# Performance work log

Measured on AMD Instinct MI355X. Metric: run time of the kernel, lower is better.

## Reference

```python
import jax, jax.numpy as jnp
import numpy as np
from jax import lax

IMAGE_SIZE = (224, 224)
NUM_NN = 3
SIGMA = 4


def _gaussian_kernel1d(sigma: float) -> jnp.ndarray:
    # anomalib/kornia: kernel_size = 2 * int(4.0 * sigma + 0.5) + 1
    ksize = 2 * int(4.0 * sigma + 0.5) + 1
    x = jnp.arange(ksize, dtype=jnp.float32) - ksize // 2
    g = jnp.exp(-(x * x) / (2.0 * sigma * sigma))
    return g / jnp.sum(g)


def _gaussian_blur(x: jnp.ndarray, sigma: float) -> jnp.ndarray:
    # x: [B, 1, H, W]; reflect 'same' padding + separable depthwise conv
    g = _gaussian_kernel1d(sigma)
    k = g.shape[0]
    pad = k // 2
    x = jnp.pad(x, ((0, 0), (0, 0), (pad, pad), (pad, pad)), mode='reflect')
    dn = ('NCHW', 'OIHW', 'NCHW')
    x = lax.conv_general_dilated(x, g.reshape(1, 1, k, 1), (1, 1), 'VALID', dimension_numbers=dn)
    x = lax.conv_general_dilated(x, g.reshape(1, 1, 1, k), (1, 1), 'VALID', dimension_numbers=dn)
    return x


def setup_inputs() -> dict:
    key = jax.random.key(0)
    distance = jax.random.uniform(key, (16, 3136, 4096), dtype=jnp.float32)
    return {"distance": distance, "scale_h": 56, "scale_w": 56}


def reference(distance, scale_h, scale_w):
    b = distance.shape[0]
    d = jnp.sqrt(distance)                                   # [B, HW, M]
    # topk smallest (ascending), like torch.topk(largest=False)
    vals = -lax.top_k(-d, NUM_NN)[0]                         # [B, HW, K]
    w = jax.nn.softmax(-vals, axis=-1)                       # softmin
    s = w[:, :, 0] * vals[:, :, 0]                           # [B, HW]
    score = s.reshape(b, 1, scale_h, scale_w)                # 'b (h w) c -> b c h w', c=1
    score = lax.stop_gradient(score)                         # .detach()
    amap = jnp.mean(score, axis=1, keepdims=True)            # [B, 1, h, w]
    amap = jax.image.resize(amap, (b, 1, IMAGE_SIZE[0], IMAGE_SIZE[1]), method='bilinear')
    return _gaussian_blur(amap, SIGMA)
```

## Files before the change

### kernel.cpp

```cpp
#include <hip/hip_runtime.h>

#define NB   16
#define HW   3136
#define MEL  4096
#define SH   56
#define SW   56
#define OH   224
#define OW   224
#define KRAD 16
#define NPIX (NB * OH * OW)

__device__ __forceinline__ void ins3(float v, float& m0, float& m1, float& m2) {
    float a = fminf(v, m0);
    float b = fmaxf(v, m0);
    m0 = a;
    float c = fminf(b, m1);
    float d = fmaxf(b, m1);
    m1 = c;
    m2 = fminf(d, m2);
}

__global__ __launch_bounds__(256) void topk_score_kernel(const float* __restrict__ dist,
                                                         float* __restrict__ score) {
    const int wid  = threadIdx.x >> 6;
    const int lane = threadIdx.x & 63;
    const long long row = (long long)blockIdx.x * 4 + wid;
    const float4* p = (const float4*)(dist + row * (long long)MEL);

    float a0 = 3.4e38f, a1 = 3.4e38f, a2 = 3.4e38f;
    float b0 = 3.4e38f, b1 = 3.4e38f, b2 = 3.4e38f;

    #pragma unroll 4
    for (int j = 0; j < 16; ++j) {
        float4 v = p[lane + 64 * j];
        ins3(v.x, a0, a1, a2);
        ins3(v.y, b0, b1, b2);
        ins3(v.z, a0, a1, a2);
        ins3(v.w, b0, b1, b2);
    }
    ins3(b0, a0, a1, a2);
    ins3(b1, a0, a1, a2);
    ins3(b2, a0, a1, a2);

    #pragma unroll
    for (int off = 32; off > 0; off >>= 1) {
        float s0 = __shfl_xor(a0, off);
        float s1 = __shfl_xor(a1, off);
        float s2 = __shfl_xor(a2, off);
        ins3(s0, a0, a1, a2);
        ins3(s1, a0, a1, a2);
        ins3(s2, a0, a1, a2);
    }

    if (lane == 0) {
        float v0 = sqrtf(a0), v1 = sqrtf(a1), v2 = sqrtf(a2);
        float e1 = expf(v0 - v1);
        float e2 = expf(v0 - v2);
        score[row] = v0 / (1.0f + e1 + e2);
    }
}

__global__ void init_gauss_kernel(float* __restrict__ g) {
    __shared__ float t[2 * KRAD + 1];
    int i = threadIdx.x;
    if (i < 2 * KRAD + 1) {
        float k = (float)(i - KRAD);
        t[i] = expf(-k * k * (1.0f / 32.0f));
    }
    __syncthreads();
    if (i == 0) {
        float s = 0.0f;
        for (int j = 0; j < 2 * KRAD + 1; ++j) s += t[j];
        for (int j = 0; j < 2 * KRAD + 1; ++j) g[j] = t[j] / s;
    }
}

__global__ __launch_bounds__(256) void upsample_kernel(const float* __restrict__ score,
                                                       float* __restrict__ out) {
    int idx = blockIdx.x * 256 + threadIdx.x;
    if (idx >= NPIX) return;
    int ox = idx % OW;
    int t  = idx / OW;
    int oy = t % OH;
    int b  = t / OH;

    float sx = (ox + 0.5f) * 0.25f - 0.5f;
    float sy = (oy + 0.5f) * 0.25f - 0.5f;
    sx = fmaxf(sx, 0.0f);
    sy = fmaxf(sy, 0.0f);
    int x0 = (int)sx;
    int y0 = (int)sy;
    float fx = sx - (float)x0;
    float fy = sy - (float)y0;
    int x1 = min(x0 + 1, SW - 1);
    int y1 = min(y0 + 1, SH - 1);

    const float* s = score + b * (SH * SW);
    float v00 = s[y0 * SW + x0];
    float v01 = s[y0 * SW + x1];
    float v10 = s[y1 * SW + x0];
    float v11 = s[y1 * SW + x1];
    float r0 = v00 + (v01 - v00) * fx;
    float r1 = v10 + (v11 - v10) * fx;
    out[idx] = r0 + (r1 - r0) * fy;
}

__global__ __launch_bounds__(256) void blur_v_kernel(const float* __restrict__ in,
                                                     const float* __restrict__ g,
                                                     float* __restrict__ out) {
    int idx = blockIdx.x * 256 + threadIdx.x;
    if (idx >= NPIX) return;
    int x = idx % OW;
    int t = idx / OW;
    int y = t % OH;
    const float* img = in + (long long)(t - y) * OW;

    float acc = 0.0f;
    #pragma unroll
    for (int k = -KRAD; k <= KRAD; ++k) {
        int yy = y + k;
        yy = (yy < 0) ? -yy : yy;
        yy = (yy > OH - 1) ? (2 * (OH - 1) - yy) : yy;
        acc += g[k + KRAD] * img[yy * OW + x];
    }
    out[idx] = acc;
}

__global__ __launch_bounds__(256) void blur_h_kernel(const float* __restrict__ in,
                                                     const float* __restrict__ g,
                                                     float* __restrict__ out) {
    int idx = blockIdx.x * 256 + threadIdx.x;
    if (idx >= NPIX) return;
    int x = idx % OW;
    const float* rowp = in + (idx - x);

    float acc = 0.0f;
    #pragma unroll
    for (int k = -KRAD; k <= KRAD; ++k) {
        int xx = x + k;
        xx = (xx < 0) ? -xx : xx;
        xx = (xx > OW - 1) ? (2 * (OW - 1) - xx) : xx;
        acc += g[k + KRAD] * rowp[xx];
    }
    out[idx] = acc;
}

extern "C" void kernel_launch(void* const* d_in, const int* in_sizes, int n_in,
                              void* d_out, int out_size, void* d_ws, size_t ws_size,
                              hipStream_t stream) {
    const float* dist = (const float*)d_in[0];
    float* out = (float*)d_out;

    char* ws = (char*)d_ws;
    float* score = (float*)ws;
    float* gauss = (float*)(ws + 50176 * 4);
    float* tmp   = (float*)(ws + 262144);

    init_gauss_kernel<<<1, 64, 0, stream>>>(gauss);
    topk_score_kernel<<<(NB * HW) / 4, 256, 0, stream>>>(dist, score);
    upsample_kernel<<<NPIX / 256, 256, 0, stream>>>(score, out);
    blur_v_kernel<<<NPIX / 256, 256, 0, stream>>>(out, gauss, tmp);
    blur_h_kernel<<<NPIX / 256, 256, 0, stream>>>(tmp, gauss, out);
}
```

Before: 171.8 us.

## Fuse upsample and separable blur into one kernel, batch nontemporal loads in top-k

The gaussian init, bilinear upsample, vertical blur and horizontal blur are merged into a single post kernel with one block per output row. Each block recomputes the upsampled values it needs straight from the small score map and keeps the row in shared memory for the horizontal pass. This removes three launches and the full-resolution intermediate buffers. The top-k kernel now issues all sixteen vector loads up front as nontemporal loads, which adds memory-level parallelism at the cost of more registers.

```diff
diff --git a/kernel.cpp b/kernel.cpp
--- a/kernel.cpp
+++ b/kernel.cpp
@@ -9,6 +9,8 @@
 #define OW   224
 #define KRAD 16
 #define NPIX (NB * OH * OW)
+
+typedef float vf4 __attribute__((ext_vector_type(4)));
 
 __device__ __forceinline__ void ins3(float v, float& m0, float& m1, float& m2) {
     float a = fminf(v, m0);
@@ -25,18 +27,22 @@
     const int wid  = threadIdx.x >> 6;
     const int lane = threadIdx.x & 63;
     const long long row = (long long)blockIdx.x * 4 + wid;
-    const float4* p = (const float4*)(dist + row * (long long)MEL);
+    const vf4* p = (const vf4*)(dist + row * (long long)MEL);
+
+    vf4 v[16];
+    #pragma unroll
+    for (int j = 0; j < 16; ++j)
+        v[j] = __builtin_nontemporal_load(p + lane + 64 * j);
 
     float a0 = 3.4e38f, a1 = 3.4e38f, a2 = 3.4e38f;
     float b0 = 3.4e38f, b1 = 3.4e38f, b2 = 3.4e38f;
 
-    #pragma unroll 4
+    #pragma unroll
     for (int j = 0; j < 16; ++j) {
-        float4 v = p[lane + 64 * j];
-        ins3(v.x, a0, a1, a2);
-        ins3(v.y, b0, b1, b2);
-        ins3(v.z, a0, a1, a2);
-        ins3(v.w, b0, b1, b2);
+        ins3(v[j][0], a0, a1, a2);
+        ins3(v[j][1], b0, b1, b2);
+        ins3(v[j][2], a0, a1, a2);
+        ins3(v[j][3], b0, b1, b2);
     }
     ins3(b0, a0, a1, a2);
     ins3(b1, a0, a1, a2);
@@ -54,95 +60,73 @@
 
     if (lane == 0) {
         float v0 = sqrtf(a0), v1 = sqrtf(a1), v2 = sqrtf(a2);
-        float e1 = expf(v0 - v1);
-        float e2 = expf(v0 - v2);
-        score[row] = v0 / (1.0f + e1 + e2);
+        score[row] = v0 / (1.0f + expf(v0 - v1) + expf(v0 - v2));
     }
 }
 
-__global__ void init_gauss_kernel(float* __restrict__ g) {
-    __shared__ float t[2 * KRAD + 1];
-    int i = threadIdx.x;
-    if (i < 2 * KRAD + 1) {
-        float k = (float)(i - KRAD);
-        t[i] = expf(-k * k * (1.0f / 32.0f));
+__global__ __launch_bounds__(256) void post_kernel(const float* __restrict__ score,
+                                                   float* __restrict__ out) {
+    __shared__ float g[2 * KRAD + 1];
+    __shared__ float row[OW];
+    __shared__ float snorm;
+
+    const int tid = threadIdx.x;
+    if (tid < 2 * KRAD + 1) {
+        float k = (float)(tid - KRAD);
+        g[tid] = expf(-k * k * (1.0f / 32.0f));
     }
     __syncthreads();
-    if (i == 0) {
+    if (tid == 0) {
         float s = 0.0f;
-        for (int j = 0; j < 2 * KRAD + 1; ++j) s += t[j];
-        for (int j = 0; j < 2 * KRAD + 1; ++j) g[j] = t[j] / s;
+        #pragma unroll
+        for (int j = 0; j < 2 * KRAD + 1; ++j) s += g[j];
+        snorm = 1.0f / (s * s);
     }
-}
 
-__global__ __launch_bounds__(256) void upsample_kernel(const float* __restrict__ score,
-                                                       float* __restrict__ out) {
-    int idx = blockIdx.x * 256 + threadIdx.x;
-    if (idx >= NPIX) return;
-    int ox = idx % OW;
-    int t  = idx / OW;
-    int oy = t % OH;
-    int b  = t / OH;
+    const int b = blockIdx.x / OH;
+    const int y = blockIdx.x % OH;
+    const float* s = score + b * (SH * SW);
+    const int x = tid;
 
-    float sx = (ox + 0.5f) * 0.25f - 0.5f;
-    float sy = (oy + 0.5f) * 0.25f - 0.5f;
-    sx = fmaxf(sx, 0.0f);
-    sy = fmaxf(sy, 0.0f);
-    int x0 = (int)sx;
-    int y0 = (int)sy;
-    float fx = sx - (float)x0;
-    float fy = sy - (float)y0;
-    int x1 = min(x0 + 1, SW - 1);
-    int y1 = min(y0 + 1, SH - 1);
+    if (x < OW) {
+        float sx = fmaxf((x + 0.5f) * 0.25f - 0.5f, 0.0f);
+        int   x0 = (int)sx;
+        float fx = sx - (float)x0;
+        int   x1 = min(x0 + 1, SW - 1);
 
-    const float* s = score + b * (SH * SW);
-    float v00 = s[y0 * SW + x0];
-    float v01 = s[y0 * SW + x1];
-    float v10 = s[y1 * SW + x0];
-    float v11 = s[y1 * SW + x1];
-    float r0 = v00 + (v01 - v00) * fx;
-    float r1 = v10 + (v11 - v10) * fx;
-    out[idx] = r0 + (r1 - r0) * fy;
-}
+        float acc = 0.0f;
+        #pragma unroll
+        for (int k = -KRAD; k <= KRAD; ++k) {
+            int yy = y + k;
+            yy = (yy < 0) ? -yy : yy;
+            yy = (yy > OH - 1) ? (2 * (OH - 1) - yy) : yy;
+            float sy = fmaxf((yy + 0.5f) * 0.25f - 0.5f, 0.0f);
+            int   y0 = (int)sy;
+            float fy = sy - (float)y0;
+            int   y1 = min(y0 + 1, SH - 1);
+            const float* r0 = s + y0 * SW;
+            const float* r1 = s + y1 * SW;
+            float v00 = r0[x0], v01 = r0[x1];
+            float v10 = r1[x0], v11 = r1[x1];
+            float e0 = v00 + (v01 - v00) * fx;
+            float e1 = v10 + (v11 - v10) * fx;
+            acc += g[k + KRAD] * (e0 + (e1 - e0) * fy);
+        }
+        row[x] = acc;
+    }
+    __syncthreads();
 
-__global__ __launch_bounds__(256) void blur_v_kernel(const float* __restrict__ in,
-                                                     const float* __restrict__ g,
-                                                     float* __restrict__ out) {
-    int idx = blockIdx.x * 256 + threadIdx.x;
-    if (idx >= NPIX) return;
-    int x = idx % OW;
-    int t = idx / OW;
-    int y = t % OH;
-    const float* img = in + (long long)(t - y) * OW;
-
-    float acc = 0.0f;
-    #pragma unroll
-    for (int k = -KRAD; k <= KRAD; ++k) {
-        int yy = y + k;
-        yy = (yy < 0) ? -yy : yy;
-        yy = (yy > OH - 1) ? (2 * (OH - 1) - yy) : yy;
-        acc += g[k + KRAD] * img[yy * OW + x];
+    if (x < OW) {
+        float acc = 0.0f;
+        #pragma unroll
+        for (int k = -KRAD; k <= KRAD; ++k) {
+            int xx = x + k;
+            xx = (xx < 0) ? -xx : xx;
+            xx = (xx > OW - 1) ? (2 * (OW - 1) - xx) : xx;
+            acc += g[k + KRAD] * row[xx];
+        }
+        out[blockIdx.x * OW + x] = acc * snorm;
     }
-    out[idx] = acc;
-}
-
-__global__ __launch_bounds__(256) void blur_h_kernel(const float* __restrict__ in,
-                                                     const float* __restrict__ g,
-                                                     float* __restrict__ out) {
-    int idx = blockIdx.x * 256 + threadIdx.x;
-    if (idx >= NPIX) return;
-    int x = idx % OW;
-    const float* rowp = in + (idx - x);
-
-    float acc = 0.0f;
-    #pragma unroll
-    for (int k = -KRAD; k <= KRAD; ++k) {
-        int xx = x + k;
-        xx = (xx < 0) ? -xx : xx;
-        xx = (xx > OW - 1) ? (2 * (OW - 1) - xx) : xx;
-        acc += g[k + KRAD] * rowp[xx];
-    }
-    out[idx] = acc;
 }
 
 extern "C" void kernel_launch(void* const* d_in, const int* in_sizes, int n_in,
@@ -150,15 +134,8 @@
                               hipStream_t stream) {
     const float* dist = (const float*)d_in[0];
     float* out = (float*)d_out;
+    float* scorebuf = (float*)d_ws;
 
-    char* ws = (char*)d_ws;
-    float* score = (float*)ws;
-    float* gauss = (float*)(ws + 50176 * 4);
-    float* tmp   = (float*)(ws + 262144);
-
-    init_gauss_kernel<<<1, 64, 0, stream>>>(gauss);
-    topk_score_kernel<<<(NB * HW) / 4, 256, 0, stream>>>(dist, score);
-    upsample_kernel<<<NPIX / 256, 256, 0, stream>>>(score, out);
-    blur_v_kernel<<<NPIX / 256, 256, 0, stream>>>(out, gauss, tmp);
-    blur_h_kernel<<<NPIX / 256, 256, 0, stream>>>(tmp, gauss, out);
+    topk_score_kernel<<<(NB * HW) / 4, 256, 0, stream>>>(dist, scorebuf);
+    post_kernel<<<NB * OH, 256, 0, stream>>>(scorebuf, out);
 }
```

Result: faster. 152.9 us (-11.0%).
